# Kernel tuning notes

Hardware: AMD Instinct MI355X
Metric: run time of the kernel (lower is better)

The kernel has to match this reference:

```python
import jax, jax.numpy as jnp
import numpy as np
from jax import lax

B, OBS, E, H = 65536, 20, 64, 64


def setup_inputs() -> dict:
    key = jax.random.key(0)
    ks = jax.random.split(key, 13)
    s = 0.1
    inp = {
        "obs_traj": jax.random.normal(ks[0], (B, OBS, 2), jnp.float32),
        "W_emb": jax.random.normal(ks[1], (E, 2), jnp.float32) * s,
        "b_emb": jax.random.normal(ks[2], (E,), jnp.float32) * s,
        "Wih_e": jax.random.normal(ks[3], (4 * H, E), jnp.float32) * s,
        "Whh_e": jax.random.normal(ks[4], (4 * H, H), jnp.float32) * s,
        "bih_e": jax.random.normal(ks[5], (4 * H,), jnp.float32) * s,
        "bhh_e": jax.random.normal(ks[6], (4 * H,), jnp.float32) * s,
        "Wih_d": jax.random.normal(ks[7], (4 * H, E), jnp.float32) * s,
        "Whh_d": jax.random.normal(ks[8], (4 * H, H), jnp.float32) * s,
        "bih_d": jax.random.normal(ks[9], (4 * H,), jnp.float32) * s,
        "bhh_d": jax.random.normal(ks[10], (4 * H,), jnp.float32) * s,
        "W_fc": jax.random.normal(ks[11], (2, H), jnp.float32) * s,
        "b_fc": jax.random.normal(ks[12], (2,), jnp.float32) * s,
        "pred_len": 12,
    }
    return inp


def _lstm_step(x, h, c, Wih, Whh, b):
    # PyTorch LSTM gate order: i, f, g, o
    g = x @ Wih.T + h @ Whh.T + b  # [B, 4H]
    i, f, gg, o = jnp.split(g, 4, axis=-1)
    c2 = jax.nn.sigmoid(f) * c + jax.nn.sigmoid(i) * jnp.tanh(gg)
    h2 = jax.nn.sigmoid(o) * jnp.tanh(c2)
    return h2, c2


def reference(obs_traj, W_emb, b_emb, Wih_e, Whh_e, bih_e, bhh_e,
              Wih_d, Whh_d, bih_d, bhh_d, W_fc, b_fc, pred_len):
    bsz = obs_traj.shape[0]
    dt = obs_traj.dtype
    # Encoder: embed all observed steps at once, then scan the LSTM over time.
    emb = jax.nn.relu(obs_traj @ W_emb.T + b_emb)  # [B, OBS, E]
    b_e = bih_e + bhh_e
    h0 = jnp.zeros((bsz, H), dt)
    c0 = jnp.zeros((bsz, H), dt)

    def enc_step(carry, x_t):
        h, c = carry
        h, c = _lstm_step(x_t, h, c, Wih_e, Whh_e, b_e)
        return (h, c), None

    (h, c), _ = lax.scan(enc_step, (h0, c0), jnp.swapaxes(emb, 0, 1))

    b_d = bih_d + bhh_d
    dec_in = jax.nn.relu(obs_traj[:, -1, :] @ W_emb.T + b_emb)  # [B, E]

    def dec_step(carry, _):
        h, c, x = carry
        h, c = _lstm_step(x, h, c, Wih_d, Whh_d, b_d)
        pred = h @ W_fc.T + b_fc  # [B, 2]
        nxt = jax.nn.relu(pred @ W_emb.T + b_emb)
        return (h, c, nxt), pred

    _, preds = lax.scan(dec_step, (h, c, dec_in), None, length=pred_len)
    return jnp.swapaxes(preds, 0, 1)  # [B, pred_len, 2]
```

## Files before the change

kernel.cpp:

```cpp
#include <hip/hip_runtime.h>

typedef __bf16 bf16x8 __attribute__((ext_vector_type(8)));
typedef __bf16 bf16x4 __attribute__((ext_vector_type(4)));
typedef float  f32x4  __attribute__((ext_vector_type(4)));
typedef float  f32x2  __attribute__((ext_vector_type(2)));

constexpr int OBS   = 20;
constexpr int PRED  = 12;
constexpr int AST   = 136;
constexpr int NBIG  = 512;
constexpr int GRID  = 768;

constexpr float SIO = -1.4426950408889634f;
constexpr float SG  =  2.8853900817779268f;

__device__ __forceinline__ float exp2_(float x) { return __builtin_amdgcn_exp2f(x); }
__device__ __forceinline__ float rcp_(float x)  { return __builtin_amdgcn_rcpf(x); }

struct SmallW {
    float  biasf_e[256];
    float  biasf_d[256];
    float4 embc[64];
    float  wfc[128];
    float  bfc[2];
};

__device__ __forceinline__ void load_bfr(bf16x8 (&bfr)[4][3],
                                         const float* Wih, const float* Whh,
                                         int wblk, int m, int q) {
    #pragma unroll
    for (int c = 0; c < 4; ++c) {
        const float sc = (c == 2) ? SG : SIO;
        const int n = c * 64 + wblk + m;
        #pragma unroll
        for (int kt = 0; kt < 3; ++kt) {
            const float* s = (kt < 2) ? (Wih + n * 64 + kt * 32 + q * 8)
                                      : (Whh + n * 64 + q * 8);
            float4 a = *(const float4*)s;
            float4 b = *(const float4*)(s + 4);
            bf16x8 v;
            v[0] = (__bf16)(sc * a.x); v[1] = (__bf16)(sc * a.y);
            v[2] = (__bf16)(sc * a.z); v[3] = (__bf16)(sc * a.w);
            v[4] = (__bf16)(sc * b.x); v[5] = (__bf16)(sc * b.y);
            v[6] = (__bf16)(sc * b.z); v[7] = (__bf16)(sc * b.w);
            bfr[c][kt] = v;
        }
    }
}

__device__ __forceinline__ void fill_wkt3(bf16x8* wkt3, const float* Whh,
                                          int wv, int lane, int wblk, int m, int q) {
    #pragma unroll
    for (int c = 0; c < 4; ++c) {
        const float sc = (c == 2) ? SG : SIO;
        const int n = c * 64 + wblk + m;
        const float* s = Whh + n * 64 + 32 + q * 8;
        float4 a = *(const float4*)s;
        float4 b = *(const float4*)(s + 4);
        bf16x8 v;
        v[0] = (__bf16)(sc * a.x); v[1] = (__bf16)(sc * a.y);
        v[2] = (__bf16)(sc * a.z); v[3] = (__bf16)(sc * a.w);
        v[4] = (__bf16)(sc * b.x); v[5] = (__bf16)(sc * b.y);
        v[6] = (__bf16)(sc * b.z); v[7] = (__bf16)(sc * b.w);
        wkt3[(wv * 4 + c) * 64 + lane] = v;
    }
}

template<int NSUB>
__device__ void lstm_body(__bf16* As, bf16x8* wkt3, SmallW& sw,
                          const float* obs,
                          const float* Wih_e, const float* Whh_e,
                          const float* Wih_d, const float* Whh_d,
                          float* out, size_t gRow0)
{
    constexpr int CH = NSUB * 16;
    constexpr int NP = (NSUB + 1) / 2;
    const int tid  = threadIdx.x;
    const int wv   = tid >> 6;
    const int lane = tid & 63;
    const int m    = lane & 15;
    const int q    = lane >> 4;
    const int wblk = wv * 16;

    bf16x8 bfr[4][3];
    load_bfr(bfr, Wih_e, Whh_e, wblk, m, q);

    f32x4 cst[2 * NSUB];
    #pragma unroll
    for (int i = 0; i < 2 * NSUB; ++i) cst[i] = f32x4{0.f, 0.f, 0.f, 0.f};

    f32x4 acc[NSUB][4];

    auto gemm = [&](int chunk, const float* bfrag) {
        #pragma unroll
        for (int c = 0; c < 4; ++c) {
            f32x4 b = *(const f32x4*)&bfrag[(wv * 4 + c) * 16 + q * 4];
            #pragma unroll
            for (int s = 0; s < NSUB; ++s) acc[s][c] = b;
        }
        #pragma unroll
        for (int kt = 0; kt < 3; ++kt) {
            bf16x8 af[NSUB];
            #pragma unroll
            for (int s = 0; s < NSUB; ++s)
                af[s] = *(const bf16x8*)&As[(chunk * CH + s * 16 + m) * AST + kt * 32 + q * 8];
            #pragma unroll
            for (int s = 0; s < NSUB; ++s)
                #pragma unroll
                for (int c = 0; c < 4; ++c)
                    acc[s][c] = __builtin_amdgcn_mfma_f32_16x16x32_bf16(bfr[c][kt], af[s], acc[s][c], 0, 0, 0);
        }
        {
            bf16x8 af[NSUB];
            #pragma unroll
            for (int s = 0; s < NSUB; ++s)
                af[s] = *(const bf16x8*)&As[(chunk * CH + s * 16 + m) * AST + 96 + q * 8];
            #pragma unroll
            for (int c = 0; c < 4; ++c) {
                bf16x8 w3 = wkt3[(wv * 4 + c) * 64 + lane];
                #pragma unroll
                for (int s = 0; s < NSUB; ++s)
                    acc[s][c] = __builtin_amdgcn_mfma_f32_16x16x32_bf16(w3, af[s], acc[s][c], 0, 0, 0);
            }
        }
    };

    auto update = [&](int chunk) {
        #pragma unroll
        for (int sub = 0; sub < NSUB; ++sub) {
            const int idx = chunk * NSUB + sub;
            const int row = chunk * CH + sub * 16 + m;
            f32x4 ci = cst[idx];
            bf16x4 h4;
            #pragma unroll
            for (int r = 0; r < 4; ++r) {
                const float gi = acc[sub][0][r];
                const float gf = acc[sub][1][r];
                const float gg = acc[sub][2][r];
                const float go = acc[sub][3][r];
                const float Ef = exp2_(gf);
                const float a  = ci[r] * rcp_(1.0f + Ef);
                const float Ei = exp2_(gi);
                const float Eg = exp2_(gg);
                const float d1 = 1.0f + Ei;
                const float r1 = rcp_(fmaf(d1, Eg, d1));
                const float cN = fmaf(Eg - 1.0f, r1, a);
                const float Eo = exp2_(go);
                const float Ec = exp2_(cN * SG);
                const float d2 = 1.0f + Eo;
                const float r2 = rcp_(fmaf(d2, Ec, d2));
                const float h  = (Ec - 1.0f) * r2;
                ci[r] = cN;
                h4[r] = (__bf16)h;
            }
            cst[idx] = ci;
            *(bf16x4*)&As[row * AST + 64 + wblk + q * 4] = h4;
        }
    };

    auto load_obs = [&](int chunk, int t, f32x2* ov) {
        #pragma unroll
        for (int p = 0; p < NP; ++p) {
            const int rloc = p * 32 + (lane & 31);
            if (rloc < CH)
                ov[p] = *(const f32x2*)(obs + (gRow0 + chunk * CH + rloc) * (OBS * 2) + t * 2);
        }
    };
    auto emb_store = [&](int chunk, const f32x2* ov) {
        const int h8 = lane >> 5;
        #pragma unroll
        for (int p = 0; p < NP; ++p) {
            const int rloc = p * 32 + (lane & 31);
            if (rloc < CH) {
                const int row = chunk * CH + rloc;
                bf16x8 v;
                #pragma unroll
                for (int j = 0; j < 8; ++j) {
                    float4 wc = sw.embc[wblk + h8 * 8 + j];
                    v[j] = (__bf16)fmaxf(fmaf(ov[p][0], wc.x, fmaf(ov[p][1], wc.y, wc.z)), 0.f);
                }
                *(bf16x8*)&As[row * AST + wblk + h8 * 8] = v;
            }
        }
    };

    __syncthreads();

    {
        f32x2 o0[NP], o1[NP];
        load_obs(0, 0, o0); load_obs(1, 0, o1);
        emb_store(0, o0);   emb_store(1, o1);
    }
    __syncthreads();
    gemm(0, sw.biasf_e);

    for (int t = 0; t < OBS; ++t) {
        __syncthreads();
        f32x2 ovA[NP];
        if (t + 1 < OBS) load_obs(0, t + 1, ovA);
        update(0);
        gemm(1, sw.biasf_e);
        if (t + 1 < OBS) emb_store(0, ovA);
        __syncthreads();
        f32x2 ovB[NP];
        if (t + 1 < OBS) load_obs(1, t + 1, ovB);
        update(1);
        if (t + 1 < OBS) {
            gemm(0, sw.biasf_e);
            emb_store(1, ovB);
        }
    }

    load_bfr(bfr, Wih_d, Whh_d, wblk, m, q);
    fill_wkt3(wkt3, Whh_d, wv, lane, wblk, m, q);

    bf16x8 wcf[2];
    {
        float4 we = sw.embc[wblk + m];
        #pragma unroll
        for (int kt = 0; kt < 2; ++kt) {
            bf16x8 v;
            #pragma unroll
            for (int j = 0; j < 8; ++j) {
                const int k = kt * 32 + q * 8 + j;
                v[j] = (__bf16)(we.x * sw.wfc[k] + we.y * sw.wfc[64 + k]);
            }
            wcf[kt] = v;
        }
    }
    f32x4 bcf;
    #pragma unroll
    for (int r = 0; r < 4; ++r) {
        float4 wc = sw.embc[wblk + q * 4 + r];
        bcf[r] = wc.x * sw.bfc[0] + wc.y * sw.bfc[1] + wc.z;
    }

    auto emb_gemm = [&](int chunk) {
        #pragma unroll
        for (int s = 0; s < NSUB; ++s) {
            const int row = chunk * CH + s * 16 + m;
            f32x4 a = bcf;
            #pragma unroll
            for (int kt = 0; kt < 2; ++kt) {
                bf16x8 hf = *(const bf16x8*)&As[row * AST + 64 + kt * 32 + q * 8];
                a = __builtin_amdgcn_mfma_f32_16x16x32_bf16(wcf[kt], hf, a, 0, 0, 0);
            }
            bf16x4 x4;
            #pragma unroll
            for (int r = 0; r < 4; ++r) x4[r] = (__bf16)fmaxf(a[r], 0.f);
            *(bf16x4*)&As[row * AST + wblk + q * 4] = x4;
        }
    };

    auto pred_phase = [&](int chunk, int td) {
        const int comp = (tid >> 2) & 1;
        const int seg  = tid & 3;
        #pragma unroll
        for (int p = 0; p < NP; ++p) {
            const int rloc = p * 32 + (tid >> 3);
            const int row  = chunk * CH + rloc;
            const bool act = (rloc < CH);
            float pv = 0.f;
            if (act) {
                bf16x8 h0 = *(const bf16x8*)&As[row * AST + 64 + seg * 16];
                bf16x8 h1 = *(const bf16x8*)&As[row * AST + 64 + seg * 16 + 8];
                f32x4 w0 = *(const f32x4*)&sw.wfc[comp * 64 + seg * 16];
                f32x4 w1 = *(const f32x4*)&sw.wfc[comp * 64 + seg * 16 + 4];
                f32x4 w2 = *(const f32x4*)&sw.wfc[comp * 64 + seg * 16 + 8];
                f32x4 w3 = *(const f32x4*)&sw.wfc[comp * 64 + seg * 16 + 12];
                pv = (float)h0[0] * w0[0] + (float)h0[1] * w0[1] + (float)h0[2] * w0[2] + (float)h0[3] * w0[3]
                   + (float)h0[4] * w1[0] + (float)h0[5] * w1[1] + (float)h0[6] * w1[2] + (float)h0[7] * w1[3]
                   + (float)h1[0] * w2[0] + (float)h1[1] * w2[1] + (float)h1[2] * w2[2] + (float)h1[3] * w2[3]
                   + (float)h1[4] * w3[0] + (float)h1[5] * w3[1] + (float)h1[6] * w3[2] + (float)h1[7] * w3[3];
            }
            pv += __shfl_xor(pv, 1, 64);
            pv += __shfl_xor(pv, 2, 64);
            if (act && seg == 0) {
                pv += sw.bfc[comp];
                out[((gRow0 + row) * PRED + td) * 2 + comp] = pv;
            }
        }
    };

    gemm(0, sw.biasf_d);

    for (int td = 0; td < PRED; ++td) {
        __syncthreads();
        update(0);
        gemm(1, sw.biasf_d);
        __syncthreads();
        update(1);
        if (td + 1 < PRED) emb_gemm(0);
        pred_phase(0, td);
        __syncthreads();
        if (td + 1 < PRED) {
            emb_gemm(1);
            gemm(0, sw.biasf_d);
        }
        pred_phase(1, td);
    }
}

__global__ __launch_bounds__(256, 3)
void vanilla_lstm(const float* __restrict__ obs,
                  const float* __restrict__ W_emb, const float* __restrict__ b_emb,
                  const float* __restrict__ Wih_e, const float* __restrict__ Whh_e,
                  const float* __restrict__ bih_e, const float* __restrict__ bhh_e,
                  const float* __restrict__ Wih_d, const float* __restrict__ Whh_d,
                  const float* __restrict__ bih_d, const float* __restrict__ bhh_d,
                  const float* __restrict__ W_fc,  const float* __restrict__ b_fc,
                  float* __restrict__ out)
{
    __shared__ __align__(16) __bf16 As[96 * AST];
    __shared__ bf16x8 wkt3[1024];
    __shared__ SmallW sw;

    const int tid = threadIdx.x;

    {
        const int wv_ = tid >> 6, c_ = (tid >> 4) & 3, qr = tid & 15;
        const int g = c_ * 64 + wv_ * 16 + qr;
        const float sc = (c_ == 2) ? SG : SIO;
        sw.biasf_e[tid] = sc * (bih_e[g] + bhh_e[g]);
        sw.biasf_d[tid] = sc * (bih_d[g] + bhh_d[g]);
    }
    if (tid < 64)  sw.embc[tid] = make_float4(W_emb[2 * tid], W_emb[2 * tid + 1], b_emb[tid], 0.f);
    if (tid < 128) sw.wfc[tid]  = W_fc[tid];
    if (tid < 2)   sw.bfc[tid]  = b_fc[tid];

    {
        uint4 z; z.x = z.y = z.z = z.w = 0u;
        #pragma unroll
        for (int i = 0; i < 3; ++i) {
            const int idx = tid + i * 256;
            const int r = idx >> 3, o = idx & 7;
            *((uint4*)&As[r * AST + 64] + o) = z;
        }
    }

    {
        const int wv = tid >> 6, lane = tid & 63, m = lane & 15, q = lane >> 4;
        fill_wkt3(wkt3, Whh_e, wv, lane, wv * 16, m, q);
    }

    const int bid = blockIdx.x;
    if (bid < NBIG) {
        lstm_body<3>(As, wkt3, sw, obs, Wih_e, Whh_e, Wih_d, Whh_d,
                     out, (size_t)bid * 96);
    } else {
        lstm_body<2>(As, wkt3, sw, obs, Wih_e, Whh_e, Wih_d, Whh_d,
                     out, (size_t)NBIG * 96 + (size_t)(bid - NBIG) * 64);
    }
}

extern "C" void kernel_launch(void* const* d_in, const int* in_sizes, int n_in,
                              void* d_out, int out_size, void* d_ws, size_t ws_size,
                              hipStream_t stream) {
    (void)in_sizes; (void)n_in; (void)d_ws; (void)ws_size; (void)out_size;
    const float* obs   = (const float*)d_in[0];
    const float* W_emb = (const float*)d_in[1];
    const float* b_emb = (const float*)d_in[2];
    const float* Wih_e = (const float*)d_in[3];
    const float* Whh_e = (const float*)d_in[4];
    const float* bih_e = (const float*)d_in[5];
    const float* bhh_e = (const float*)d_in[6];
    const float* Wih_d = (const float*)d_in[7];
    const float* Whh_d = (const float*)d_in[8];
    const float* bih_d = (const float*)d_in[9];
    const float* bhh_d = (const float*)d_in[10];
    const float* W_fc  = (const float*)d_in[11];
    const float* b_fc  = (const float*)d_in[12];
    float* o = (float*)d_out;

    dim3 grid(GRID), block(256);
    hipLaunchKernelGGL(vanilla_lstm, grid, block, 0, stream,
                       obs, W_emb, b_emb, Wih_e, Whh_e, bih_e, bhh_e,
                       Wih_d, Whh_d, bih_d, bhh_d, W_fc, b_fc, o);
}
```

Measured before the change: 271.8 us.

## Interleave per-subtile LSTM gate updates with MFMA gemms and use MFMA for predictions

The chunk-wide gemm and update lambdas are split into per-16-row subtile versions, and each subtile's gate math is interleaved with the next chunk's MFMA work so transcendental ALU ops can overlap matrix instructions. The cell-update math is reworked to use a single reciprocal for the forget/input/g gates instead of two. The decoder's scalar dot-product prediction with shuffles is replaced by a pair of MFMAs on a zero-padded W_fc fragment, fused with the embedding gemm. This adds register pressure from the extra fragments and a combined reciprocal whose product of three terms could overflow for large gate values.

```diff
diff --git a/kernel.cpp b/kernel.cpp
--- a/kernel.cpp
+++ b/kernel.cpp
@@ -91,71 +91,57 @@
 
     f32x4 acc[NSUB][4];
 
-    auto gemm = [&](int chunk, const float* bfrag) {
-        #pragma unroll
-        for (int c = 0; c < 4; ++c) {
-            f32x4 b = *(const f32x4*)&bfrag[(wv * 4 + c) * 16 + q * 4];
-            #pragma unroll
-            for (int s = 0; s < NSUB; ++s) acc[s][c] = b;
-        }
+    auto gemm_sub = [&](int chunk, int s, const float* bfrag) {
+        const int rowb = (chunk * CH + s * 16 + m) * AST;
+        #pragma unroll
+        for (int c = 0; c < 4; ++c)
+            acc[s][c] = *(const f32x4*)&bfrag[(wv * 4 + c) * 16 + q * 4];
         #pragma unroll
         for (int kt = 0; kt < 3; ++kt) {
-            bf16x8 af[NSUB];
-            #pragma unroll
-            for (int s = 0; s < NSUB; ++s)
-                af[s] = *(const bf16x8*)&As[(chunk * CH + s * 16 + m) * AST + kt * 32 + q * 8];
-            #pragma unroll
-            for (int s = 0; s < NSUB; ++s)
-                #pragma unroll
-                for (int c = 0; c < 4; ++c)
-                    acc[s][c] = __builtin_amdgcn_mfma_f32_16x16x32_bf16(bfr[c][kt], af[s], acc[s][c], 0, 0, 0);
+            bf16x8 af = *(const bf16x8*)&As[rowb + kt * 32 + q * 8];
+            #pragma unroll
+            for (int c = 0; c < 4; ++c)
+                acc[s][c] = __builtin_amdgcn_mfma_f32_16x16x32_bf16(bfr[c][kt], af, acc[s][c], 0, 0, 0);
         }
         {
-            bf16x8 af[NSUB];
-            #pragma unroll
-            for (int s = 0; s < NSUB; ++s)
-                af[s] = *(const bf16x8*)&As[(chunk * CH + s * 16 + m) * AST + 96 + q * 8];
+            bf16x8 af = *(const bf16x8*)&As[rowb + 96 + q * 8];
             #pragma unroll
             for (int c = 0; c < 4; ++c) {
                 bf16x8 w3 = wkt3[(wv * 4 + c) * 64 + lane];
-                #pragma unroll
-                for (int s = 0; s < NSUB; ++s)
-                    acc[s][c] = __builtin_amdgcn_mfma_f32_16x16x32_bf16(w3, af[s], acc[s][c], 0, 0, 0);
+                acc[s][c] = __builtin_amdgcn_mfma_f32_16x16x32_bf16(w3, af, acc[s][c], 0, 0, 0);
             }
         }
     };
 
-    auto update = [&](int chunk) {
-        #pragma unroll
-        for (int sub = 0; sub < NSUB; ++sub) {
-            const int idx = chunk * NSUB + sub;
-            const int row = chunk * CH + sub * 16 + m;
-            f32x4 ci = cst[idx];
-            bf16x4 h4;
-            #pragma unroll
-            for (int r = 0; r < 4; ++r) {
-                const float gi = acc[sub][0][r];
-                const float gf = acc[sub][1][r];
-                const float gg = acc[sub][2][r];
-                const float go = acc[sub][3][r];
-                const float Ef = exp2_(gf);
-                const float a  = ci[r] * rcp_(1.0f + Ef);
-                const float Ei = exp2_(gi);
-                const float Eg = exp2_(gg);
-                const float d1 = 1.0f + Ei;
-                const float r1 = rcp_(fmaf(d1, Eg, d1));
-                const float cN = fmaf(Eg - 1.0f, r1, a);
-                const float Eo = exp2_(go);
-                const float Ec = exp2_(cN * SG);
-                const float d2 = 1.0f + Eo;
-                const float r2 = rcp_(fmaf(d2, Ec, d2));
-                const float h  = (Ec - 1.0f) * r2;
-                ci[r] = cN;
-                h4[r] = (__bf16)h;
-            }
-            cst[idx] = ci;
-            *(bf16x4*)&As[row * AST + 64 + wblk + q * 4] = h4;
-        }
+    auto update_sub = [&](int chunk, int s) {
+        const int idx = chunk * NSUB + s;
+        const int row = chunk * CH + s * 16 + m;
+        f32x4 ci = cst[idx];
+        bf16x4 h4;
+        #pragma unroll
+        for (int r = 0; r < 4; ++r) {
+            const float gi = acc[s][0][r];
+            const float gf = acc[s][1][r];
+            const float gg = acc[s][2][r];
+            const float go = acc[s][3][r];
+            const float Ef = exp2_(gf);
+            const float Ei = exp2_(gi);
+            const float Eg = exp2_(gg);
+            const float pf = 1.0f + Ef;
+            const float t1 = (1.0f + Ei) * (1.0f + Eg);
+            const float R  = rcp_(pf * t1);
+            const float num = fmaf(ci[r], t1, (Eg - 1.0f) * pf);
+            const float cN = num * R;
+            const float Eo = exp2_(go);
+            const float Ec = exp2_(cN * SG);
+            const float d2 = 1.0f + Eo;
+            const float r2 = rcp_(fmaf(d2, Ec, d2));
+            const float h  = (Ec - 1.0f) * r2;
+            ci[r] = cN;
+            h4[r] = (__bf16)h;
+        }
+        cst[idx] = ci;
+        *(bf16x4*)&As[row * AST + 64 + wblk + q * 4] = h4;
     };
 
     auto load_obs = [&](int chunk, int t, f32x2* ov) {
@@ -192,23 +178,28 @@
         emb_store(0, o0);   emb_store(1, o1);
     }
     __syncthreads();
-    gemm(0, sw.biasf_e);
+    #pragma unroll
+    for (int s = 0; s < NSUB; ++s) gemm_sub(0, s, sw.biasf_e);
 
     for (int t = 0; t < OBS; ++t) {
         __syncthreads();
         f32x2 ovA[NP];
         if (t + 1 < OBS) load_obs(0, t + 1, ovA);
-        update(0);
-        gemm(1, sw.biasf_e);
+        #pragma unroll
+        for (int s = 0; s < NSUB; ++s) {
+            update_sub(0, s);
+            gemm_sub(1, s, sw.biasf_e);
+        }
         if (t + 1 < OBS) emb_store(0, ovA);
         __syncthreads();
         f32x2 ovB[NP];
         if (t + 1 < OBS) load_obs(1, t + 1, ovB);
-        update(1);
-        if (t + 1 < OBS) {
-            gemm(0, sw.biasf_e);
-            emb_store(1, ovB);
-        }
+        #pragma unroll
+        for (int s = 0; s < NSUB; ++s) {
+            update_sub(1, s);
+            if (t + 1 < OBS) gemm_sub(0, s, sw.biasf_e);
+        }
+        if (t + 1 < OBS) emb_store(1, ovB);
     }
 
     load_bfr(bfr, Wih_d, Whh_d, wblk, m, q);
@@ -234,70 +225,66 @@
         float4 wc = sw.embc[wblk + q * 4 + r];
         bcf[r] = wc.x * sw.bfc[0] + wc.y * sw.bfc[1] + wc.z;
     }
-
-    auto emb_gemm = [&](int chunk) {
-        #pragma unroll
-        for (int s = 0; s < NSUB; ++s) {
-            const int row = chunk * CH + s * 16 + m;
+    bf16x8 wfcf[2];
+    #pragma unroll
+    for (int kt = 0; kt < 2; ++kt) {
+        bf16x8 v;
+        #pragma unroll
+        for (int j = 0; j < 8; ++j) v[j] = (__bf16)0.f;
+        if (m < 2) {
+            #pragma unroll
+            for (int j = 0; j < 8; ++j)
+                v[j] = (__bf16)sw.wfc[m * 64 + kt * 32 + q * 8 + j];
+        }
+        wfcf[kt] = v;
+    }
+    const float bfc0 = sw.bfc[0], bfc1 = sw.bfc[1];
+
+    auto embpred_sub = [&](int chunk, int s, int td, bool doEmb) {
+        const int row = chunk * CH + s * 16 + m;
+        bf16x8 hf0 = *(const bf16x8*)&As[row * AST + 64 + q * 8];
+        bf16x8 hf1 = *(const bf16x8*)&As[row * AST + 96 + q * 8];
+        if (doEmb) {
             f32x4 a = bcf;
-            #pragma unroll
-            for (int kt = 0; kt < 2; ++kt) {
-                bf16x8 hf = *(const bf16x8*)&As[row * AST + 64 + kt * 32 + q * 8];
-                a = __builtin_amdgcn_mfma_f32_16x16x32_bf16(wcf[kt], hf, a, 0, 0, 0);
-            }
+            a = __builtin_amdgcn_mfma_f32_16x16x32_bf16(wcf[0], hf0, a, 0, 0, 0);
+            a = __builtin_amdgcn_mfma_f32_16x16x32_bf16(wcf[1], hf1, a, 0, 0, 0);
             bf16x4 x4;
             #pragma unroll
             for (int r = 0; r < 4; ++r) x4[r] = (__bf16)fmaxf(a[r], 0.f);
             *(bf16x4*)&As[row * AST + wblk + q * 4] = x4;
         }
-    };
-
-    auto pred_phase = [&](int chunk, int td) {
-        const int comp = (tid >> 2) & 1;
-        const int seg  = tid & 3;
-        #pragma unroll
-        for (int p = 0; p < NP; ++p) {
-            const int rloc = p * 32 + (tid >> 3);
-            const int row  = chunk * CH + rloc;
-            const bool act = (rloc < CH);
-            float pv = 0.f;
-            if (act) {
-                bf16x8 h0 = *(const bf16x8*)&As[row * AST + 64 + seg * 16];
-                bf16x8 h1 = *(const bf16x8*)&As[row * AST + 64 + seg * 16 + 8];
-                f32x4 w0 = *(const f32x4*)&sw.wfc[comp * 64 + seg * 16];
-                f32x4 w1 = *(const f32x4*)&sw.wfc[comp * 64 + seg * 16 + 4];
-                f32x4 w2 = *(const f32x4*)&sw.wfc[comp * 64 + seg * 16 + 8];
-                f32x4 w3 = *(const f32x4*)&sw.wfc[comp * 64 + seg * 16 + 12];
-                pv = (float)h0[0] * w0[0] + (float)h0[1] * w0[1] + (float)h0[2] * w0[2] + (float)h0[3] * w0[3]
-                   + (float)h0[4] * w1[0] + (float)h0[5] * w1[1] + (float)h0[6] * w1[2] + (float)h0[7] * w1[3]
-                   + (float)h1[0] * w2[0] + (float)h1[1] * w2[1] + (float)h1[2] * w2[2] + (float)h1[3] * w2[3]
-                   + (float)h1[4] * w3[0] + (float)h1[5] * w3[1] + (float)h1[6] * w3[2] + (float)h1[7] * w3[3];
-            }
-            pv += __shfl_xor(pv, 1, 64);
-            pv += __shfl_xor(pv, 2, 64);
-            if (act && seg == 0) {
-                pv += sw.bfc[comp];
-                out[((gRow0 + row) * PRED + td) * 2 + comp] = pv;
-            }
-        }
-    };
-
-    gemm(0, sw.biasf_d);
+        if (wv == s) {
+            f32x4 p = f32x4{bfc0, bfc1, 0.f, 0.f};
+            p = __builtin_amdgcn_mfma_f32_16x16x32_bf16(wfcf[0], hf0, p, 0, 0, 0);
+            p = __builtin_amdgcn_mfma_f32_16x16x32_bf16(wfcf[1], hf1, p, 0, 0, 0);
+            if (q == 0)
+                *(f32x2*)&out[((gRow0 + row) * PRED + td) * 2] = f32x2{p[0], p[1]};
+        }
+    };
+
+    #pragma unroll
+    for (int s = 0; s < NSUB; ++s) gemm_sub(0, s, sw.biasf_d);
 
     for (int td = 0; td < PRED; ++td) {
-        __syncthreads();
-        update(0);
-        gemm(1, sw.biasf_d);
-        __syncthreads();
-        update(1);
-        if (td + 1 < PRED) emb_gemm(0);
-        pred_phase(0, td);
-        __syncthreads();
-        if (td + 1 < PRED) {
-            emb_gemm(1);
-            gemm(0, sw.biasf_d);
-        }
-        pred_phase(1, td);
+        const bool more = (td + 1 < PRED);
+        __syncthreads();
+        #pragma unroll
+        for (int s = 0; s < NSUB; ++s) {
+            update_sub(0, s);
+            gemm_sub(1, s, sw.biasf_d);
+        }
+        __syncthreads();
+        #pragma unroll
+        for (int s = 0; s < NSUB; ++s) {
+            update_sub(1, s);
+            embpred_sub(0, s, td, more);
+        }
+        __syncthreads();
+        #pragma unroll
+        for (int s = 0; s < NSUB; ++s) {
+            embpred_sub(1, s, td, more);
+            if (more) gemm_sub(0, s, sw.biasf_d);
+        }
     }
 }
 
```

New measurement: 307.4 us. +13.1%, slower.
